# Kernel tuning notes

Measured on AMD Instinct MI355X. Metric: run time of the kernel, lower is better.

The kernel has to match this reference:

```python
import jax, jax.numpy as jnp
import numpy as np

D_MODEL = 768; D_STATE = 16; D_CONV = 4; EXPAND = 2
D_INNER = EXPAND * D_MODEL          # 1536
DT_RANK = (D_MODEL + 15) // 16      # 48 (mamba_ssm default dt_rank='auto')
BATCH = 2; SEQ = 2048
LN_EPS = 1e-5


def setup_inputs() -> dict:
    key = jax.random.key(0)
    ks = iter(jax.random.split(key, 64))
    def rn(shape, scale=0.02):
        return jax.random.normal(next(ks), shape, jnp.float32) * scale
    inp = {"x": jax.random.normal(next(ks), (BATCH, SEQ, D_MODEL), jnp.float32)}
    for p in ("f", "b"):
        inp[p + "_in_w"]    = rn((2 * D_INNER, D_MODEL))
        inp[p + "_conv_w"]  = rn((D_INNER, D_CONV), 0.2)
        inp[p + "_conv_b"]  = jnp.zeros((D_INNER,), jnp.float32)
        inp[p + "_xproj_w"] = rn((DT_RANK + 2 * D_STATE, D_INNER))
        inp[p + "_dt_w"]    = rn((D_INNER, DT_RANK), 0.1)
        inp[p + "_dt_b"]    = rn((D_INNER,), 0.1)
        inp[p + "_A_log"]   = jnp.log(jnp.broadcast_to(
            jnp.arange(1, D_STATE + 1, dtype=jnp.float32), (D_INNER, D_STATE)))
        inp[p + "_D"]       = jnp.ones((D_INNER,), jnp.float32)
        inp[p + "_out_w"]   = rn((D_MODEL, D_INNER))
    inp["ln1_g"] = jnp.ones((D_MODEL,), jnp.float32)
    inp["ln1_b"] = jnp.zeros((D_MODEL,), jnp.float32)
    inp["ln2_g"] = jnp.ones((D_MODEL,), jnp.float32)
    inp["ln2_b"] = jnp.zeros((D_MODEL,), jnp.float32)
    inp["ff_w1"] = rn((4 * D_MODEL, D_MODEL))
    inp["ff_b1"] = jnp.zeros((4 * D_MODEL,), jnp.float32)
    inp["ff_w2"] = rn((D_MODEL, 4 * D_MODEL))
    inp["ff_b2"] = jnp.zeros((D_MODEL,), jnp.float32)
    return inp


def _layernorm(x, g, b):
    mu = jnp.mean(x, -1, keepdims=True)
    var = jnp.mean((x - mu) ** 2, -1, keepdims=True)
    return (x - mu) * jax.lax.rsqrt(var + LN_EPS) * g + b


def _selective_scan(u, dt, A, Bm, Cm, Dp):
    # u, dt: [B,L,Dh]; A: [Dh,N]; Bm, Cm: [B,L,N]; Dp: [Dh]
    uT, dtT = jnp.swapaxes(u, 0, 1), jnp.swapaxes(dt, 0, 1)   # time-major
    BmT, CmT = jnp.swapaxes(Bm, 0, 1), jnp.swapaxes(Cm, 0, 1)
    h0 = jnp.zeros((u.shape[0], u.shape[2], A.shape[1]), u.dtype)  # [B,Dh,N]
    def step(h, inp):
        u_t, dt_t, b_t, c_t = inp
        dA = jnp.exp(dt_t[:, :, None] * A)                        # [B,Dh,N]
        h = h * dA + (dt_t * u_t)[:, :, None] * b_t[:, None, :]
        return h, jnp.einsum('bdn,bn->bd', h, c_t)
    _, ys = jax.lax.scan(step, h0, (uT, dtT, BmT, CmT))
    return jnp.swapaxes(ys, 0, 1) + u * Dp


def _mamba(x, in_w, conv_w, conv_b, xproj_w, dt_w, dt_b, A_log, Dp, out_w):
    xz = x @ in_w.T                              # [B,L,2*Dh]
    xh, z = jnp.split(xz, 2, axis=-1)
    # causal depthwise conv over time
    xc = jnp.swapaxes(xh, 1, 2)                  # [B,Dh,L]
    xc = jnp.pad(xc, ((0, 0), (0, 0), (D_CONV - 1, 0)))
    xc = jax.lax.conv_general_dilated(xc, conv_w[:, None, :], (1,), 'VALID',
                                      feature_group_count=D_INNER)
    xh = jax.nn.silu(jnp.swapaxes(xc + conv_b[None, :, None], 1, 2))
    x_dbl = xh @ xproj_w.T                       # [B,L,dt_rank+2N]
    dt, Bm, Cm = jnp.split(x_dbl, [DT_RANK, DT_RANK + D_STATE], axis=-1)
    dt = jax.nn.softplus(dt @ dt_w.T + dt_b)     # [B,L,Dh]
    A = -jnp.exp(A_log)                          # [Dh,N]
    y = _selective_scan(xh, dt, A, Bm, Cm, Dp)
    return (y * jax.nn.silu(z)) @ out_w.T


def _forward(x, f_in_w, f_conv_w, f_conv_b, f_xproj_w, f_dt_w, f_dt_b, f_A_log,
             f_D, f_out_w, b_in_w, b_conv_w, b_conv_b, b_xproj_w, b_dt_w, b_dt_b,
             b_A_log, b_D, b_out_w, ln1_g, ln1_b, ln2_g, ln2_b,
             ff_w1, ff_b1, ff_w2, ff_b2):
    xn = _layernorm(x, ln1_g, ln1_b)
    fo = _mamba(xn, f_in_w, f_conv_w, f_conv_b, f_xproj_w, f_dt_w, f_dt_b,
                f_A_log, f_D, f_out_w)
    bo = _mamba(xn[:, ::-1], b_in_w, b_conv_w, b_conv_b, b_xproj_w, b_dt_w,
                b_dt_b, b_A_log, b_D, b_out_w)[:, ::-1]
    m = _layernorm(fo + bo, ln2_g, ln2_b)
    ff = jax.nn.gelu(m @ ff_w1.T + ff_b1, approximate=False) @ ff_w2.T + ff_b2
    return ff + x


def reference(x, f_in_w, f_conv_w, f_conv_b, f_xproj_w, f_dt_w, f_dt_b, f_A_log,
              f_D, f_out_w, b_in_w, b_conv_w, b_conv_b, b_xproj_w, b_dt_w, b_dt_b,
              b_A_log, b_D, b_out_w, ln1_g, ln1_b, ln2_g, ln2_b,
              ff_w1, ff_b1, ff_w2, ff_b2):
    return _forward(x, f_in_w, f_conv_w, f_conv_b, f_xproj_w, f_dt_w, f_dt_b,
                    f_A_log, f_D, f_out_w, b_in_w, b_conv_w, b_conv_b, b_xproj_w,
                    b_dt_w, b_dt_b, b_A_log, b_D, b_out_w, ln1_g, ln1_b, ln2_g,
                    ln2_b, ff_w1, ff_b1, ff_w2, ff_b2)
```

## Files before the change

### kernel.cpp

```cpp
#include <hip/hip_runtime.h>
#include <cstdint>
#include <cstddef>

#define BATCH_ 2
#define SEQ_ 2048
#define DM 768
#define DH 1536
#define NS 16
#define RK 48
#define MR (BATCH_*SEQ_)
#define NCH 32
#define CL (SEQ_/NCH)
#define NCHAN (2*BATCH_*DH)
#define NDBLK (DH/256)

typedef __attribute__((ext_vector_type(8))) short short8b;
typedef __attribute__((ext_vector_type(4))) float f32x4;
typedef __attribute__((address_space(1))) const unsigned int gas_u32;
typedef __attribute__((address_space(3))) unsigned int las_u32;

__device__ __forceinline__ float sigmoidf_(float x){ return 1.f/(1.f+__expf(-x)); }

__device__ __forceinline__ void split1(float x, ushort& h, ushort& l){
  unsigned u = __float_as_uint(x);
  h = (ushort)(u >> 16);
  float lf = x - __uint_as_float(u & 0xFFFF0000u);
  l = (ushort)(__float_as_uint(lf) >> 16);
}

__global__ __launch_bounds__(256) void split_kernel(const float* __restrict__ in,
    ushort* __restrict__ hi, ushort* __restrict__ lo, int n4)
{
  int i = blockIdx.x*256 + threadIdx.x;
  if (i >= n4) return;
  float4 v = ((const float4*)in)[i];
  ushort h0,h1,h2,h3,l0,l1,l2,l3;
  split1(v.x,h0,l0); split1(v.y,h1,l1); split1(v.z,h2,l2); split1(v.w,h3,l3);
  ((ushort4*)hi)[i] = make_ushort4(h0,h1,h2,h3);
  ((ushort4*)lo)[i] = make_ushort4(l0,l1,l2,l3);
}

__global__ __launch_bounds__(256) void ln1_kernel(const float* __restrict__ x,
    const float* __restrict__ g, const float* __restrict__ bta,
    ushort* __restrict__ xnh, ushort* __restrict__ xnl)
{
  int row = blockIdx.x;
  int tid = threadIdx.x;
  __shared__ float s1[256], s2[256];
  float v[3]; float sum=0.f, sq=0.f;
  const float* xr = x + (size_t)row*DM;
  #pragma unroll
  for (int i=0;i<3;i++){ v[i] = xr[tid + i*256]; sum += v[i]; sq += v[i]*v[i]; }
  s1[tid]=sum; s2[tid]=sq; __syncthreads();
  for (int off=128; off>0; off>>=1){
    if (tid<off){ s1[tid]+=s1[tid+off]; s2[tid]+=s2[tid+off]; }
    __syncthreads();
  }
  float mean = s1[0] * (1.f/DM);
  float var  = s2[0] * (1.f/DM) - mean*mean;
  float rstd = rsqrtf(var + 1e-5f);
  #pragma unroll
  for (int i=0;i<3;i++){
    int c = tid + i*256;
    float val = (v[i]-mean)*rstd*g[c] + bta[c];
    ushort h, lo_;
    split1(val, h, lo_);
    xnh[(size_t)row*DM + c] = h;  xnl[(size_t)row*DM + c] = lo_;
  }
}

__global__ __launch_bounds__(256) void ln2_kernel(const float* __restrict__ fo,
    const float* __restrict__ bo, const float* __restrict__ g,
    const float* __restrict__ bta, ushort* __restrict__ mh, ushort* __restrict__ ml)
{
  int row = blockIdx.x;
  int tid = threadIdx.x;
  int bb = row >> 11, l = row & (SEQ_-1);
  __shared__ float s1[256], s2[256];
  size_t rrow = ((size_t)bb*SEQ_ + (SEQ_-1-l))*DM;
  float v[3]; float sum=0.f, sq=0.f;
  #pragma unroll
  for (int i=0;i<3;i++){
    int c = tid + i*256;
    v[i] = fo[(size_t)row*DM + c] + bo[rrow + c];
    sum += v[i]; sq += v[i]*v[i];
  }
  s1[tid]=sum; s2[tid]=sq; __syncthreads();
  for (int off=128; off>0; off>>=1){
    if (tid<off){ s1[tid]+=s1[tid+off]; s2[tid]+=s2[tid+off]; }
    __syncthreads();
  }
  float mean = s1[0] * (1.f/DM);
  float var  = s2[0] * (1.f/DM) - mean*mean;
  float rstd = rsqrtf(var + 1e-5f);
  #pragma unroll
  for (int i=0;i<3;i++){
    int c = tid + i*256;
    float val = (v[i]-mean)*rstd*g[c] + bta[c];
    ushort h, lo_;
    split1(val, h, lo_);
    mh[(size_t)row*DM + c] = h;  ml[(size_t)row*DM + c] = lo_;
  }
}

template<int ACT, bool RAW>
__global__ __launch_bounds__(256) void gemm_nt(const float* __restrict__ A, int lda,
    const float* __restrict__ W, const float* __restrict__ bias,
    float* __restrict__ C, int ldc, const float* __restrict__ res,
    int M, int N, int K, int Kc)
{
  __shared__ float As[16][64];
  __shared__ float Ws[16][64];
  int tid = threadIdx.x;
  int tx = tid & 15, ty = tid >> 4;
  int m0 = blockIdx.y * 64, n0 = blockIdx.x * 64;
  int lm = tid >> 2;
  int lk = (tid & 3) * 4;
  const int kbeg = RAW ? blockIdx.z*Kc : 0;
  const int kend = RAW ? kbeg + Kc : K;
  float acc[4][4] = {};
  for (int k0 = kbeg; k0 < kend; k0 += 16) {
    float4 av = *(const float4*)(A + (size_t)(m0+lm)*lda + k0 + lk);
    As[lk+0][lm] = av.x; As[lk+1][lm] = av.y; As[lk+2][lm] = av.z; As[lk+3][lm] = av.w;
    int wn = n0 + lm;
    float4 wv = make_float4(0.f,0.f,0.f,0.f);
    if (wn < N) wv = *(const float4*)(W + (size_t)wn*K + k0 + lk);
    Ws[lk+0][lm] = wv.x; Ws[lk+1][lm] = wv.y; Ws[lk+2][lm] = wv.z; Ws[lk+3][lm] = wv.w;
    __syncthreads();
    #pragma unroll
    for (int k = 0; k < 16; ++k) {
      float4 a = *(const float4*)&As[k][ty*4];
      float4 w = *(const float4*)&Ws[k][tx*4];
      acc[0][0] += a.x*w.x; acc[0][1] += a.x*w.y; acc[0][2] += a.x*w.z; acc[0][3] += a.x*w.w;
      acc[1][0] += a.y*w.x; acc[1][1] += a.y*w.y; acc[1][2] += a.y*w.z; acc[1][3] += a.y*w.w;
      acc[2][0] += a.z*w.x; acc[2][1] += a.z*w.y; acc[2][2] += a.z*w.z; acc[2][3] += a.z*w.w;
      acc[3][0] += a.w*w.x; acc[3][1] += a.w*w.y; acc[3][2] += a.w*w.z; acc[3][3] += a.w*w.w;
    }
    __syncthreads();
  }
  if constexpr (RAW){
    float* P = C + (size_t)blockIdx.z*((size_t)M*N);
    #pragma unroll
    for (int i=0;i<4;i++){
      int row = m0 + ty*4 + i;
      #pragma unroll
      for (int j=0;j<4;j++){
        int col = n0 + tx*4 + j;
        if (col < N) P[(size_t)row*N + col] = acc[i][j];
      }
    }
  } else {
    #pragma unroll
    for (int i=0;i<4;i++){
      int row = m0 + ty*4 + i;
      #pragma unroll
      for (int j=0;j<4;j++){
        int col = n0 + tx*4 + j;
        if (col < N) {
          float vv = acc[i][j];
          if (bias) vv += bias[col];
          if (ACT == 1) vv = (vv > 20.f) ? vv : log1pf(expf(vv));
          if (res) vv += res[(size_t)row*ldc + col];
          C[(size_t)row*ldc + col] = vv;
        }
      }
    }
  }
}

template<int ACT, int OUT, bool REV>
__global__ __launch_bounds__(256,3) void gemm_mfma(
    const ushort* __restrict__ Ah_g, const ushort* __restrict__ Al_g, int ldaA,
    const ushort* __restrict__ Wh_g, const ushort* __restrict__ Wl_g,
    const float* __restrict__ bias, float* __restrict__ C,
    ushort* __restrict__ Oh, ushort* __restrict__ Ol,
    int ldc, const float* __restrict__ res,
    int M, int N, int K, int Kc)
{
  __shared__ short8b L[2048];
  const int tid = threadIdx.x;
  const int m0 = blockIdx.y*128, n0 = blockIdx.x*128;
  const int lane = tid & 63, wv = tid >> 6;
  const int wr = (wv>>1)*64, wc = (wv&1)*64;
  const int li = lane & 15, lg = lane >> 4;
  const int kbeg = (OUT==1) ? blockIdx.z*Kc : 0;
  const int nkt = ((OUT==1) ? Kc : K) >> 5;

  const int lr8 = lane >> 3, ls = lane & 7;
  const int sl = ls ^ lr8;
  const int chunk = (sl & 3) * 8;
  const ushort* gA = (sl < 4) ? Ah_g : Al_g;
  const ushort* gB = (sl < 4) ? Wh_g : Wl_g;
  const ushort* aAddr[4]; const ushort* bAddr[4];
  #pragma unroll
  for (int i=0;i<4;i++){
    int rg = m0 + wv*32 + i*8 + lr8;
    if constexpr (REV) rg ^= (SEQ_-1);
    aAddr[i] = gA + (size_t)rg*ldaA + kbeg + chunk;
    int rb = n0 + wv*32 + i*8 + lr8;
    bAddr[i] = gB + (size_t)rb*K + kbeg + chunk;
  }

  f32x4 acc[4][4];
  #pragma unroll
  for (int i=0;i<4;i++)
    #pragma unroll
    for (int j=0;j<4;j++) acc[i][j] = (f32x4){0.f,0.f,0.f,0.f};

  for (int kt=0; kt<nkt; ++kt){
    const int ko = kt*32;
    #pragma unroll
    for (int i=0;i<4;i++){
      __builtin_amdgcn_global_load_lds((gas_u32*)(aAddr[i]+ko),
          (las_u32*)&L[(wv*32+i*8)*8], 16, 0, 0);
      __builtin_amdgcn_global_load_lds((gas_u32*)(bAddr[i]+ko),
          (las_u32*)&L[1024+(wv*32+i*8)*8], 16, 0, 0);
    }
    __syncthreads();
    short8b afh[4],afl[4],bfh[4],bfl[4];
    #pragma unroll
    for (int f=0; f<4; f++){
      int sa = (wr+f*16+li)*8 + (lg ^ (li&7));
      int sb = 1024 + (wc+f*16+li)*8 + (lg ^ (li&7));
      afh[f]=L[sa]; afl[f]=L[sa^4];
      bfh[f]=L[sb]; bfl[f]=L[sb^4];
    }
    #pragma unroll
    for (int fr=0;fr<4;fr++)
      #pragma unroll
      for (int fc=0;fc<4;fc++){
        acc[fr][fc]=__builtin_amdgcn_mfma_f32_16x16x32_bf16(afh[fr],bfh[fc],acc[fr][fc],0,0,0);
        acc[fr][fc]=__builtin_amdgcn_mfma_f32_16x16x32_bf16(afh[fr],bfl[fc],acc[fr][fc],0,0,0);
        acc[fr][fc]=__builtin_amdgcn_mfma_f32_16x16x32_bf16(afl[fr],bfh[fc],acc[fr][fc],0,0,0);
      }
    __syncthreads();
  }

  if constexpr (OUT==1){
    float* P = C + (size_t)blockIdx.z*((size_t)M*N);
    #pragma unroll
    for (int fr=0;fr<4;fr++)
      #pragma unroll
      for (int fc=0;fc<4;fc++){
        int col = n0 + wc + fc*16 + li;
        int row = m0 + wr + fr*16 + lg*4;
        #pragma unroll
        for (int rg=0;rg<4;rg++)
          P[(size_t)(row+rg)*N + col] = acc[fr][fc][rg];
      }
  } else if constexpr (OUT==2){
    #pragma unroll
    for (int fr=0;fr<4;fr++)
      #pragma unroll
      for (int fc=0;fc<4;fc++){
        int col = n0 + wc + fc*16 + li;
        int row = m0 + wr + fr*16 + lg*4;
        float bv = bias ? bias[col] : 0.f;
        #pragma unroll
        for (int rg=0;rg<4;rg++){
          float t = acc[fr][fc][rg] + bv;
          t = 0.5f*t*(1.f+erff(t*0.70710678118654752f));
          ushort h, lo_;
          split1(t, h, lo_);
          Oh[(size_t)(row+rg)*ldc + col] = h;
          Ol[(size_t)(row+rg)*ldc + col] = lo_;
        }
      }
  } else {
    #pragma unroll
    for (int fr=0;fr<4;fr++)
      #pragma unroll
      for (int fc=0;fc<4;fc++){
        int col = n0 + wc + fc*16 + li;
        int row = m0 + wr + fr*16 + lg*4;
        float bv = bias ? bias[col] : 0.f;
        #pragma unroll
        for (int rg=0;rg<4;rg++){
          float t = acc[fr][fc][rg] + bv;
          if (res) t += res[(size_t)(row+rg)*ldc + col];
          C[(size_t)(row+rg)*ldc + col] = t;
        }
      }
  }
}

__global__ __launch_bounds__(256) void reduce_split(const float* __restrict__ P,
    const float* __restrict__ bias, const float* __restrict__ res,
    float* __restrict__ C, int N, size_t elems, int nsplit)
{
  size_t i = ((size_t)blockIdx.x*256 + threadIdx.x)*4;
  float4 s = *(const float4*)(P + i);
  for (int k=1;k<nsplit;k++){
    float4 p = *(const float4*)(P + (size_t)k*elems + i);
    s.x+=p.x; s.y+=p.y; s.z+=p.z; s.w+=p.w;
  }
  if (bias){
    int col = (int)(i % (size_t)N);
    const float4 b = *(const float4*)(bias + col);
    s.x+=b.x; s.y+=b.y; s.z+=b.z; s.w+=b.w;
  }
  if (res){
    const float4 r = *(const float4*)(res + i);
    s.x+=r.x; s.y+=r.y; s.z+=r.z; s.w+=r.w;
  }
  *(float4*)(C + i) = s;
}

__global__ __launch_bounds__(256) void conv_silu_kernel(const float* __restrict__ xz,
    const float* __restrict__ cw, const float* __restrict__ cb, float* __restrict__ xh)
{
  int idx = blockIdx.x*256 + threadIdx.x;
  int d = idx % DH;
  int row = idx / DH;
  int l = row & (SEQ_-1);
  const float* base = xz + (size_t)row*(2*DH) + d;
  float acc = cb[d];
  #pragma unroll
  for (int j=0;j<4;j++){
    int ll = l - 3 + j;
    if (ll >= 0) acc += cw[d*4+j] * base[(ptrdiff_t)(j-3)*(2*DH)];
  }
  xh[(size_t)row*DH + d] = acc * sigmoidf_(acc);
}

__global__ __launch_bounds__(256) void scan_p1_kernel(
    const float* __restrict__ dt0, const float* __restrict__ xh0, const float* __restrict__ xd0,
    const float* __restrict__ Al0,
    const float* __restrict__ dt1, const float* __restrict__ xh1, const float* __restrict__ xd1,
    const float* __restrict__ Al1,
    float* __restrict__ hend, float* __restrict__ dtsum)
{
  int tid = threadIdx.x;
  int bid = blockIdx.x;
  int dblk = bid % NDBLK;
  int t   = bid / NDBLK;
  int c   = t & (NCH-1);
  int db  = t >> 5;
  int dir = db >> 1, bb = db & 1;
  int d = dblk*256 + tid;
  const float* dt = dir ? dt1 : dt0;
  const float* xh = dir ? xh1 : xh0;
  const float* xd = dir ? xd1 : xd0;
  const float* Al = dir ? Al1 : Al0;

  __shared__ float sB[CL][NS];
  {
    const float* xdb = xd + ((size_t)bb*SEQ_ + (size_t)c*CL)*80 + RK;
    int row = tid >> 2, part = tid & 3;
    *(float4*)&sB[row][part*4] = *(const float4*)(xdb + (size_t)row*80 + part*4);
  }
  float An[NS];
  {
    const float4* ap = (const float4*)(Al + (size_t)d*NS);
    #pragma unroll
    for (int q=0;q<4;q++){
      float4 a = ap[q];
      An[4*q+0] = -__expf(a.x); An[4*q+1] = -__expf(a.y);
      An[4*q+2] = -__expf(a.z); An[4*q+3] = -__expf(a.w);
    }
  }
  __syncthreads();

  float h[NS];
  #pragma unroll
  for (int n=0;n<NS;n++) h[n] = 0.f;
  float dts = 0.f;
  size_t base = ((size_t)bb*SEQ_ + (size_t)c*CL)*DH + d;
  #pragma unroll 4
  for (int l=0;l<CL;++l){
    float dtv = dt[base], uv = xh[base];
    float du = dtv*uv;
    float Bv[NS];
    *(float4*)&Bv[0]  = *(const float4*)&sB[l][0];
    *(float4*)&Bv[4]  = *(const float4*)&sB[l][4];
    *(float4*)&Bv[8]  = *(const float4*)&sB[l][8];
    *(float4*)&Bv[12] = *(const float4*)&sB[l][12];
    #pragma unroll
    for (int n=0;n<NS;n++)
      h[n] = h[n]*__expf(dtv*An[n]) + du*Bv[n];
    dts += dtv;
    base += DH;
  }
  size_t unit = ((size_t)db*DH + d)*NCH + c;
  float4* hp = (float4*)(hend + unit*NS);
  hp[0] = make_float4(h[0],h[1],h[2],h[3]);
  hp[1] = make_float4(h[4],h[5],h[6],h[7]);
  hp[2] = make_float4(h[8],h[9],h[10],h[11]);
  hp[3] = make_float4(h[12],h[13],h[14],h[15]);
  dtsum[(size_t)c*NCHAN + (size_t)db*DH + d] = dts;
}

__global__ __launch_bounds__(256) void scan_p2_kernel(
    const float* __restrict__ Al0, const float* __restrict__ Al1,
    float* __restrict__ hend, const float* __restrict__ dtsum)
{
  int t = blockIdx.x*256 + threadIdx.x;
  int n = t & 15;
  int ch = t >> 4;
  int d  = ch % DH;
  int dir = (ch / DH) >> 1;
  const float* Al = dir ? Al1 : Al0;
  float An = -__expf(Al[d*NS + n]);
  float h0 = 0.f;
  size_t ub = (size_t)ch * NCH;
  #pragma unroll
  for (int c = 0; c < NCH; ++c) {
    float P  = __expf(An * dtsum[(size_t)c*NCHAN + ch]);
    float he = hend[(ub + c)*NS + n];
    hend[(ub + c)*NS + n] = h0;
    h0 = h0 * P + he;
  }
}

__global__ __launch_bounds__(256) void scan_p3_kernel(
    const float* __restrict__ dt0, const float* __restrict__ xh0, const float* __restrict__ xd0,
    const float* __restrict__ z0, const float* __restrict__ Al0, const float* __restrict__ Dp0,
    ushort* __restrict__ yg0,
    const float* __restrict__ dt1, const float* __restrict__ xh1, const float* __restrict__ xd1,
    const float* __restrict__ z1, const float* __restrict__ Al1, const float* __restrict__ Dp1,
    ushort* __restrict__ yg1,
    const float* __restrict__ hstart)
{
  int tid = threadIdx.x;
  int bid = blockIdx.x;
  int dblk = bid % NDBLK;
  int t   = bid / NDBLK;
  int c   = t & (NCH-1);
  int db  = t >> 5;
  int dir = db >> 1, bb = db & 1;
  int d = dblk*256 + tid;
  const float* dt = dir ? dt1 : dt0;
  const float* xh = dir ? xh1 : xh0;
  const float* xd = dir ? xd1 : xd0;
  const float* zp = dir ? z1  : z0;
  const float* Al = dir ? Al1 : Al0;
  const float* Dp = dir ? Dp1 : Dp0;
  ushort*      yg = dir ? yg1 : yg0;

  __shared__ float sBC[CL][2*NS];
  {
    const float* xdb = xd + ((size_t)bb*SEQ_ + (size_t)c*CL)*80 + RK;
    #pragma unroll
    for (int i=0;i<2;i++){
      int idx = tid + i*256;
      int row = idx >> 3, part = idx & 7;
      *(float4*)&sBC[row][part*4] = *(const float4*)(xdb + (size_t)row*80 + part*4);
    }
  }
  float An[NS];
  {
    const float4* ap = (const float4*)(Al + (size_t)d*NS);
    #pragma unroll
    for (int q=0;q<4;q++){
      float4 a = ap[q];
      An[4*q+0] = -__expf(a.x); An[4*q+1] = -__expf(a.y);
      An[4*q+2] = -__expf(a.z); An[4*q+3] = -__expf(a.w);
    }
  }
  float Dd = Dp[d];
  __syncthreads();

  size_t unit = ((size_t)db*DH + d)*NCH + c;
  float h[NS];
  {
    const float4* hp = (const float4*)(hstart + unit*NS);
    float4 h0=hp[0], h1=hp[1], h2=hp[2], h3=hp[3];
    h[0]=h0.x; h[1]=h0.y; h[2]=h0.z; h[3]=h0.w;
    h[4]=h1.x; h[5]=h1.y; h[6]=h1.z; h[7]=h1.w;
    h[8]=h2.x; h[9]=h2.y; h[10]=h2.z; h[11]=h2.w;
    h[12]=h3.x; h[13]=h3.y; h[14]=h3.z; h[15]=h3.w;
  }
  size_t base = ((size_t)bb*SEQ_ + (size_t)c*CL)*DH + d;
  size_t zidx = ((size_t)bb*SEQ_ + (size_t)c*CL)*(size_t)(2*DH) + DH + d;
  size_t yrow = ((size_t)bb*SEQ_ + (size_t)c*CL)*(size_t)(4*DH) + d;
  #pragma unroll 2
  for (int l=0;l<CL;++l){
    float dtv = dt[base], uv = xh[base];
    float zv = zp[zidx];
    float du = dtv*uv;
    float Bv[NS], Cv[NS];
    *(float4*)&Bv[0]  = *(const float4*)&sBC[l][0];
    *(float4*)&Bv[4]  = *(const float4*)&sBC[l][4];
    *(float4*)&Bv[8]  = *(const float4*)&sBC[l][8];
    *(float4*)&Bv[12] = *(const float4*)&sBC[l][12];
    *(float4*)&Cv[0]  = *(const float4*)&sBC[l][16];
    *(float4*)&Cv[4]  = *(const float4*)&sBC[l][20];
    *(float4*)&Cv[8]  = *(const float4*)&sBC[l][24];
    *(float4*)&Cv[12] = *(const float4*)&sBC[l][28];
    float y = 0.f;
    #pragma unroll
    for (int n=0;n<NS;n++){
      h[n] = h[n]*__expf(dtv*An[n]) + du*Bv[n];
      y = fmaf(h[n], Cv[n], y);
    }
    float yv = (y + uv*Dd) * (zv * sigmoidf_(zv));
    ushort hh, ll;
    split1(yv, hh, ll);
    yg[yrow] = hh; yg[yrow + DH] = ll;
    base += DH; zidx += 2*DH; yrow += 4*DH;
  }
}

template<int ACT>
static inline void launch_gemm(const float* A, int lda, const float* W, const float* bias,
                               float* C, int ldc, const float* res,
                               int M, int N, int K, hipStream_t s)
{
  dim3 grid((N+63)/64, M/64);
  gemm_nt<ACT,false><<<grid, dim3(256), 0, s>>>(A, lda, W, bias, C, ldc, res, M, N, K, 0);
}

static inline void launch_gemm_splitk(const float* A, int lda, const float* W,
                                      float* P, int M, int N, int K, int nsplit,
                                      hipStream_t s)
{
  dim3 grid((N+63)/64, M/64, nsplit);
  gemm_nt<0,true><<<grid, dim3(256), 0, s>>>(A, lda, W, nullptr, P, N, nullptr,
                                             M, N, K, K/nsplit);
}

extern "C" void kernel_launch(void* const* d_in, const int* in_sizes, int n_in,
                              void* d_out, int out_size, void* d_ws, size_t ws_size,
                              hipStream_t stream)
{
  const float* x        = (const float*)d_in[0];
  const float* f_in_w   = (const float*)d_in[1];
  const float* f_conv_w = (const float*)d_in[2];
  const float* f_conv_b = (const float*)d_in[3];
  const float* f_xproj  = (const float*)d_in[4];
  const float* f_dt_w   = (const float*)d_in[5];
  const float* f_dt_b   = (const float*)d_in[6];
  const float* f_A_log  = (const float*)d_in[7];
  const float* f_D      = (const float*)d_in[8];
  const float* f_out_w  = (const float*)d_in[9];
  const float* b_in_w   = (const float*)d_in[10];
  const float* b_conv_w = (const float*)d_in[11];
  const float* b_conv_b = (const float*)d_in[12];
  const float* b_xproj  = (const float*)d_in[13];
  const float* b_dt_w   = (const float*)d_in[14];
  const float* b_dt_b   = (const float*)d_in[15];
  const float* b_A_log  = (const float*)d_in[16];
  const float* b_D      = (const float*)d_in[17];
  const float* b_out_w  = (const float*)d_in[18];
  const float* ln1_g    = (const float*)d_in[19];
  const float* ln1_b    = (const float*)d_in[20];
  const float* ln2_g    = (const float*)d_in[21];
  const float* ln2_b    = (const float*)d_in[22];
  const float* ff_w1    = (const float*)d_in[23];
  const float* ff_b1    = (const float*)d_in[24];
  const float* ff_w2    = (const float*)d_in[25];
  const float* ff_b2    = (const float*)d_in[26];
  float* out = (float*)d_out;

  float* ws = (float*)d_ws;
  size_t o = 0;
  float* xz_f   = ws + o; o += (size_t)MR*2*DH;
  float* xz_b   = ws + o; o += (size_t)MR*2*DH;
  float* xh_f   = ws + o; o += (size_t)MR*DH;
  float* xh_b   = ws + o; o += (size_t)MR*DH;
  float* xdbl_f = ws + o; o += (size_t)MR*80;
  float* xdbl_b = ws + o; o += (size_t)MR*80;
  float* dtb_f  = ws + o; o += (size_t)MR*DH;
  float* dtb_b  = ws + o; o += (size_t)MR*DH;
  float* xnbf   = ws + o; o += (size_t)MR*DM;
  float* dtsum  = ws + o; o += (size_t)NCHAN*NCH;
  float* wbf    = ws + o; o += (size_t)2*(2*DH*DM);

  ushort* xnh = (ushort*)xnbf;
  ushort* xnl = xnh + (size_t)MR*DM;
  ushort* yg_f = (ushort*)xz_f;
  ushort* yg_b = (ushort*)xz_b;
  ushort* wreg = (ushort*)wbf;
  ushort* f_inh = wreg;                       ushort* f_inl = wreg + (size_t)2*DH*DM;
  ushort* b_inh = wreg + (size_t)2*(2*DH*DM); ushort* b_inl = wreg + (size_t)3*(2*DH*DM);
  ushort* f_oth = wreg;                       ushort* f_otl = wreg + (size_t)DM*DH;
  ushort* b_oth = wreg + (size_t)2*DM*DH;     ushort* b_otl = wreg + (size_t)3*DM*DH;
  ushort* w1h   = wreg;                       ushort* w1l   = wreg + (size_t)4*DM*DM;
  ushort* w2h   = wreg + (size_t)2*(4*DM*DM); ushort* w2l   = wreg + (size_t)3*(4*DM*DM);
  float* hend  = xnbf;
  float* partX = xnbf;
  ushort* mh   = (ushort*)xh_f;
  ushort* ml   = mh + (size_t)MR*DM;
  float* fo    = xh_b;
  float* bo    = xh_b + (size_t)MR*DM;
  float* part1 = dtb_f;
  ushort* ffhh = (ushort*)dtb_f;
  ushort* ffhl = ffhh + (size_t)MR*4*DM;
  float* part2 = xz_b;
  const size_t EL = (size_t)MR*DM;
  const size_t EL2 = (size_t)MR*80;

  split_kernel<<<(2*DH*DM/4+255)/256, 256, 0, stream>>>(f_in_w, f_inh, f_inl, 2*DH*DM/4);
  split_kernel<<<(2*DH*DM/4+255)/256, 256, 0, stream>>>(b_in_w, b_inh, b_inl, 2*DH*DM/4);
  ln1_kernel<<<MR, 256, 0, stream>>>(x, ln1_g, ln1_b, xnh, xnl);
  {
    dim3 grid((2*DH)/128, MR/128);
    gemm_mfma<0,0,false><<<grid, dim3(256), 0, stream>>>(xnh, xnl, DM, f_inh, f_inl,
        nullptr, xz_f, nullptr, nullptr, 2*DH, nullptr, MR, 2*DH, DM, 0);
    gemm_mfma<0,0,true><<<grid, dim3(256), 0, stream>>>(xnh, xnl, DM, b_inh, b_inl,
        nullptr, xz_b, nullptr, nullptr, 2*DH, nullptr, MR, 2*DH, DM, 0);
  }
  split_kernel<<<(DM*DH/4+255)/256, 256, 0, stream>>>(f_out_w, f_oth, f_otl, DM*DH/4);
  split_kernel<<<(DM*DH/4+255)/256, 256, 0, stream>>>(b_out_w, b_oth, b_otl, DM*DH/4);
  conv_silu_kernel<<<(MR*DH)/256, 256, 0, stream>>>(xz_f, f_conv_w, f_conv_b, xh_f);
  conv_silu_kernel<<<(MR*DH)/256, 256, 0, stream>>>(xz_b, b_conv_w, b_conv_b, xh_b);
  launch_gemm_splitk(xh_f, DH, f_xproj, partX, MR, 80, DH, 8, stream);
  reduce_split<<<(int)(EL2/1024), 256, 0, stream>>>(partX, nullptr, nullptr, xdbl_f, 80, EL2, 8);
  launch_gemm_splitk(xh_b, DH, b_xproj, partX, MR, 80, DH, 8, stream);
  reduce_split<<<(int)(EL2/1024), 256, 0, stream>>>(partX, nullptr, nullptr, xdbl_b, 80, EL2, 8);
  launch_gemm<1>(xdbl_f, 80, f_dt_w, f_dt_b, dtb_f, DH, nullptr, MR, DH, RK, stream);
  launch_gemm<1>(xdbl_b, 80, b_dt_w, b_dt_b, dtb_b, DH, nullptr, MR, DH, RK, stream);
  scan_p1_kernel<<<4*NCH*NDBLK, 256, 0, stream>>>(
      dtb_f, xh_f, xdbl_f, f_A_log,
      dtb_b, xh_b, xdbl_b, b_A_log,
      hend, dtsum);
  scan_p2_kernel<<<(NCHAN*NS)/256, 256, 0, stream>>>(f_A_log, b_A_log, hend, dtsum);
  scan_p3_kernel<<<4*NCH*NDBLK, 256, 0, stream>>>(
      dtb_f, xh_f, xdbl_f, xz_f, f_A_log, f_D, yg_f,
      dtb_b, xh_b, xdbl_b, xz_b, b_A_log, b_D, yg_b,
      hend);
  {
    dim3 grid(DM/128, MR/128, 4);
    gemm_mfma<0,1,false><<<grid, dim3(256), 0, stream>>>(yg_f, yg_f + DH, 4*DH,
        f_oth, f_otl, nullptr, part1, nullptr, nullptr, DM, nullptr, MR, DM, DH, DH/4);
    reduce_split<<<(int)(EL/1024), 256, 0, stream>>>(part1, nullptr, nullptr, fo, DM, EL, 4);
    gemm_mfma<0,1,false><<<grid, dim3(256), 0, stream>>>(yg_b, yg_b + DH, 4*DH,
        b_oth, b_otl, nullptr, part1, nullptr, nullptr, DM, nullptr, MR, DM, DH, DH/4);
    reduce_split<<<(int)(EL/1024), 256, 0, stream>>>(part1, nullptr, nullptr, bo, DM, EL, 4);
  }
  split_kernel<<<(4*DM*DM/4+255)/256, 256, 0, stream>>>(ff_w1, w1h, w1l, 4*DM*DM/4);
  split_kernel<<<(4*DM*DM/4+255)/256, 256, 0, stream>>>(ff_w2, w2h, w2l, 4*DM*DM/4);
  ln2_kernel<<<MR, 256, 0, stream>>>(fo, bo, ln2_g, ln2_b, mh, ml);
  {
    dim3 grid1((4*DM)/128, MR/128);
    gemm_mfma<2,2,false><<<grid1, dim3(256), 0, stream>>>(mh, ml, DM, w1h, w1l,
        ff_b1, nullptr, ffhh, ffhl, 4*DM, nullptr, MR, 4*DM, DM, 0);
    dim3 grid2(DM/128, MR/128, 4);
    gemm_mfma<0,1,false><<<grid2, dim3(256), 0, stream>>>(ffhh, ffhl, 4*DM, w2h, w2l,
        nullptr, part2, nullptr, nullptr, DM, nullptr, MR, DM, 4*DM, (4*DM)/4);
    reduce_split<<<(int)(EL/1024), 256, 0, stream>>>(part2, ff_b2, x, out, DM, EL, 4);
  }
}
```

Before: 771.4 us.

## Double-buffer GEMM LDS tiles and merge forward/backward in-projection launches

The MFMA GEMM now uses two LDS buffers, so the global-to-LDS load of the next K tile is issued before the MFMAs on the current tile, overlapping memory latency with compute. The forward and backward in-projection GEMMs are merged into one launch over a z dimension of two, with z selecting the weights, the output buffer and the sequence-reversal mask at runtime. LDS use doubles and launch bounds drop from 3 to 2 blocks per CU, which may lower occupancy. The REV template parameter becomes a runtime XOR mask.

Measured after the change: 779.0 us. About the same (+1.0%).

```diff
diff --git a/kernel.cpp b/kernel.cpp
--- a/kernel.cpp
+++ b/kernel.cpp
@@ -168,34 +168,43 @@
   }
 }
 
-template<int ACT, int OUT, bool REV>
-__global__ __launch_bounds__(256,3) void gemm_mfma(
+template<int ACT, int OUT>
+__global__ __launch_bounds__(256,2) void gemm_mfma(
     const ushort* __restrict__ Ah_g, const ushort* __restrict__ Al_g, int ldaA,
     const ushort* __restrict__ Wh_g, const ushort* __restrict__ Wl_g,
+    const ushort* __restrict__ Wh2, const ushort* __restrict__ Wl2,
+    float* __restrict__ C2,
     const float* __restrict__ bias, float* __restrict__ C,
     ushort* __restrict__ Oh, ushort* __restrict__ Ol,
     int ldc, const float* __restrict__ res,
     int M, int N, int K, int Kc)
 {
-  __shared__ short8b L[2048];
+  __shared__ short8b L[2][2048];
   const int tid = threadIdx.x;
   const int m0 = blockIdx.y*128, n0 = blockIdx.x*128;
   const int lane = tid & 63, wv = tid >> 6;
   const int wr = (wv>>1)*64, wc = (wv&1)*64;
   const int li = lane & 15, lg = lane >> 4;
-  const int kbeg = (OUT==1) ? blockIdx.z*Kc : 0;
+  const int z = blockIdx.z;
+  const int kbeg = (OUT==1) ? z*Kc : 0;
   const int nkt = ((OUT==1) ? Kc : K) >> 5;
+
+  const ushort* WhS = Wh_g; const ushort* WlS = Wl_g;
+  float* Cd = C;
+  int revmask = 0;
+  if constexpr (OUT==3){
+    if (z==1){ WhS = Wh2; WlS = Wl2; Cd = C2; revmask = SEQ_-1; }
+  }
 
   const int lr8 = lane >> 3, ls = lane & 7;
   const int sl = ls ^ lr8;
   const int chunk = (sl & 3) * 8;
   const ushort* gA = (sl < 4) ? Ah_g : Al_g;
-  const ushort* gB = (sl < 4) ? Wh_g : Wl_g;
+  const ushort* gB = (sl < 4) ? WhS : WlS;
   const ushort* aAddr[4]; const ushort* bAddr[4];
   #pragma unroll
   for (int i=0;i<4;i++){
-    int rg = m0 + wv*32 + i*8 + lr8;
-    if constexpr (REV) rg ^= (SEQ_-1);
+    int rg = (m0 + wv*32 + i*8 + lr8) ^ revmask;
     aAddr[i] = gA + (size_t)rg*ldaA + kbeg + chunk;
     int rb = n0 + wv*32 + i*8 + lr8;
     bAddr[i] = gB + (size_t)rb*K + kbeg + chunk;
@@ -207,23 +216,29 @@
     #pragma unroll
     for (int j=0;j<4;j++) acc[i][j] = (f32x4){0.f,0.f,0.f,0.f};
 
+  #define STAGE_(kt_, b_) { \
+    const int ko_ = (kt_)*32; \
+    _Pragma("unroll") \
+    for (int i=0;i<4;i++){ \
+      __builtin_amdgcn_global_load_lds((gas_u32*)(aAddr[i]+ko_), \
+          (las_u32*)&L[b_][(wv*32+i*8)*8], 16, 0, 0); \
+      __builtin_amdgcn_global_load_lds((gas_u32*)(bAddr[i]+ko_), \
+          (las_u32*)&L[b_][1024+(wv*32+i*8)*8], 16, 0, 0); \
+    } }
+
+  STAGE_(0, 0);
+  __syncthreads();
+
   for (int kt=0; kt<nkt; ++kt){
-    const int ko = kt*32;
-    #pragma unroll
-    for (int i=0;i<4;i++){
-      __builtin_amdgcn_global_load_lds((gas_u32*)(aAddr[i]+ko),
-          (las_u32*)&L[(wv*32+i*8)*8], 16, 0, 0);
-      __builtin_amdgcn_global_load_lds((gas_u32*)(bAddr[i]+ko),
-          (las_u32*)&L[1024+(wv*32+i*8)*8], 16, 0, 0);
-    }
-    __syncthreads();
+    const int cur = kt & 1;
+    if (kt+1 < nkt) STAGE_(kt+1, cur^1);
     short8b afh[4],afl[4],bfh[4],bfl[4];
     #pragma unroll
     for (int f=0; f<4; f++){
       int sa = (wr+f*16+li)*8 + (lg ^ (li&7));
       int sb = 1024 + (wc+f*16+li)*8 + (lg ^ (li&7));
-      afh[f]=L[sa]; afl[f]=L[sa^4];
-      bfh[f]=L[sb]; bfl[f]=L[sb^4];
+      afh[f]=L[cur][sa]; afl[f]=L[cur][sa^4];
+      bfh[f]=L[cur][sb]; bfl[f]=L[cur][sb^4];
     }
     #pragma unroll
     for (int fr=0;fr<4;fr++)
@@ -235,9 +250,10 @@
       }
     __syncthreads();
   }
+  #undef STAGE_
 
   if constexpr (OUT==1){
-    float* P = C + (size_t)blockIdx.z*((size_t)M*N);
+    float* P = C + (size_t)z*((size_t)M*N);
     #pragma unroll
     for (int fr=0;fr<4;fr++)
       #pragma unroll
@@ -278,7 +294,7 @@
         for (int rg=0;rg<4;rg++){
           float t = acc[fr][fc][rg] + bv;
           if (res) t += res[(size_t)(row+rg)*ldc + col];
-          C[(size_t)(row+rg)*ldc + col] = t;
+          Cd[(size_t)(row+rg)*ldc + col] = t;
         }
       }
   }
@@ -594,11 +610,10 @@
   split_kernel<<<(2*DH*DM/4+255)/256, 256, 0, stream>>>(b_in_w, b_inh, b_inl, 2*DH*DM/4);
   ln1_kernel<<<MR, 256, 0, stream>>>(x, ln1_g, ln1_b, xnh, xnl);
   {
-    dim3 grid((2*DH)/128, MR/128);
-    gemm_mfma<0,0,false><<<grid, dim3(256), 0, stream>>>(xnh, xnl, DM, f_inh, f_inl,
-        nullptr, xz_f, nullptr, nullptr, 2*DH, nullptr, MR, 2*DH, DM, 0);
-    gemm_mfma<0,0,true><<<grid, dim3(256), 0, stream>>>(xnh, xnl, DM, b_inh, b_inl,
-        nullptr, xz_b, nullptr, nullptr, 2*DH, nullptr, MR, 2*DH, DM, 0);
+    dim3 grid((2*DH)/128, MR/128, 2);
+    gemm_mfma<0,3><<<grid, dim3(256), 0, stream>>>(xnh, xnl, DM, f_inh, f_inl,
+        b_inh, b_inl, xz_b, nullptr, xz_f, nullptr, nullptr, 2*DH, nullptr,
+        MR, 2*DH, DM, 0);
   }
   split_kernel<<<(DM*DH/4+255)/256, 256, 0, stream>>>(f_out_w, f_oth, f_otl, DM*DH/4);
   split_kernel<<<(DM*DH/4+255)/256, 256, 0, stream>>>(b_out_w, b_oth, b_otl, DM*DH/4);
@@ -621,11 +636,13 @@
       hend);
   {
     dim3 grid(DM/128, MR/128, 4);
-    gemm_mfma<0,1,false><<<grid, dim3(256), 0, stream>>>(yg_f, yg_f + DH, 4*DH,
-        f_oth, f_otl, nullptr, part1, nullptr, nullptr, DM, nullptr, MR, DM, DH, DH/4);
+    gemm_mfma<0,1><<<grid, dim3(256), 0, stream>>>(yg_f, yg_f + DH, 4*DH,
+        f_oth, f_otl, nullptr, nullptr, nullptr, nullptr, part1, nullptr, nullptr,
+        DM, nullptr, MR, DM, DH, DH/4);
     reduce_split<<<(int)(EL/1024), 256, 0, stream>>>(part1, nullptr, nullptr, fo, DM, EL, 4);
-    gemm_mfma<0,1,false><<<grid, dim3(256), 0, stream>>>(yg_b, yg_b + DH, 4*DH,
-        b_oth, b_otl, nullptr, part1, nullptr, nullptr, DM, nullptr, MR, DM, DH, DH/4);
+    gemm_mfma<0,1><<<grid, dim3(256), 0, stream>>>(yg_b, yg_b + DH, 4*DH,
+        b_oth, b_otl, nullptr, nullptr, nullptr, nullptr, part1, nullptr, nullptr,
+        DM, nullptr, MR, DM, DH, DH/4);
     reduce_split<<<(int)(EL/1024), 256, 0, stream>>>(part1, nullptr, nullptr, bo, DM, EL, 4);
   }
   split_kernel<<<(4*DM*DM/4+255)/256, 256, 0, stream>>>(ff_w1, w1h, w1l, 4*DM*DM/4);
@@ -633,11 +650,13 @@
   ln2_kernel<<<MR, 256, 0, stream>>>(fo, bo, ln2_g, ln2_b, mh, ml);
   {
     dim3 grid1((4*DM)/128, MR/128);
-    gemm_mfma<2,2,false><<<grid1, dim3(256), 0, stream>>>(mh, ml, DM, w1h, w1l,
-        ff_b1, nullptr, ffhh, ffhl, 4*DM, nullptr, MR, 4*DM, DM, 0);
+    gemm_mfma<2,2><<<grid1, dim3(256), 0, stream>>>(mh, ml, DM, w1h, w1l,
+        nullptr, nullptr, nullptr, ff_b1, nullptr, ffhh, ffhl, 4*DM, nullptr,
+        MR, 4*DM, DM, 0);
     dim3 grid2(DM/128, MR/128, 4);
-    gemm_mfma<0,1,false><<<grid2, dim3(256), 0, stream>>>(ffhh, ffhl, 4*DM, w2h, w2l,
-        nullptr, part2, nullptr, nullptr, DM, nullptr, MR, DM, 4*DM, (4*DM)/4);
+    gemm_mfma<0,1><<<grid2, dim3(256), 0, stream>>>(ffhh, ffhl, 4*DM, w2h, w2l,
+        nullptr, nullptr, nullptr, nullptr, part2, nullptr, nullptr,
+        DM, nullptr, MR, DM, 4*DM, (4*DM)/4);
     reduce_split<<<(int)(EL/1024), 256, 0, stream>>>(part2, ff_b2, x, out, DM, EL, 4);
   }
 }
```
